# Kernel tuning notes

Measured on AMD Instinct MI355X. Metric: run time of the kernel, lower is better.

## Reference

```python
import jax, jax.numpy as jnp
import numpy as np

S = 64.0   # margin_loss scale
M2 = 0.5   # arcface additive angular margin (m1=1.0, m3=0.0)
EPS = 1e-7

BATCH = 1024
EMB = 512
NUM_CLASSES = 200000


def setup_inputs() -> dict:
    key = jax.random.key(0)
    k1, k2, k3 = jax.random.split(key, 3)
    embeddings = jax.random.normal(k1, (BATCH, EMB), dtype=jnp.float32)
    weight = jax.random.normal(k2, (NUM_CLASSES, EMB), dtype=jnp.float32) * 0.01
    labels = jax.random.randint(k3, (BATCH,), 0, NUM_CLASSES, dtype=jnp.int64)
    return {"embeddings": embeddings, "weight": weight, "labels": labels}


def reference(embeddings, weight, labels):
    # L2 normalize rows (torch.nn.functional.normalize, eps=1e-12)
    ne = embeddings / jnp.maximum(jnp.linalg.norm(embeddings, axis=1, keepdims=True), 1e-12)
    nw = weight / jnp.maximum(jnp.linalg.norm(weight, axis=1, keepdims=True), 1e-12)
    # cosine logits [B, C], clamped to [-1, 1]
    logits = jnp.clip(jnp.einsum('be,ce->bc', ne, nw), -1.0, 1.0)
    B = logits.shape[0]
    rows = jnp.arange(B)
    lbl = labels.astype(jnp.int32)
    # arcface margin: cos(theta + m2) applied only at the target class
    target = logits[rows, lbl]
    final_target = jnp.cos(jnp.arccos(jnp.clip(target, -1.0 + EPS, 1.0 - EPS)) + M2)
    logits = logits.at[rows, lbl].set(final_target) * S
    # mean cross-entropy
    logp = jax.nn.log_softmax(logits, axis=1)
    return -jnp.mean(logp[rows, lbl])
```

## Files before the change

### kernel.cpp

```cpp
#include <hip/hip_runtime.h>
#include <math.h>


#define S_SCALE 64.0f
#define MARGIN2 0.5f
#define EPSS 1e-7f

#define BATCH 1024
#define EMB 512
#define NCLS 200000

#define BM 256
#define BN 128
#define BK 32
#define NCHUNKS ((NCLS + BN - 1) / BN)
#define LDSTR 40

typedef __bf16 bf16x8 __attribute__((ext_vector_type(8)));
typedef float floatx4 __attribute__((ext_vector_type(4)));

#define OFF_NEBF 0
#define LEN_NEBF (BATCH * EMB / 2)
#define OFF_WINV (OFF_NEBF + LEN_NEBF)
#define LEN_WINV 200192
#define OFF_PM (OFF_WINV + LEN_WINV)
#define LEN_P (BATCH * NCHUNKS)
#define OFF_PL (OFF_PM + LEN_P)
#define OFF_TSV (OFF_PL + LEN_P)
#define OFF_RL (OFF_TSV + BATCH)

__device__ inline ushort f2bf(float f) {
    unsigned u = __float_as_uint(f);
    unsigned r = (u + 0x7FFFu + ((u >> 16) & 1u)) >> 16;
    return (ushort)r;
}

__global__ void norm_emb_kernel(const float* __restrict__ e, ushort* __restrict__ nebf) {
    int r = blockIdx.x;
    int t = threadIdx.x;
    float v0 = e[r * EMB + t];
    float v1 = e[r * EMB + t + 256];
    __shared__ float red[256];
    red[t] = v0 * v0 + v1 * v1;
    __syncthreads();
    for (int o = 128; o > 0; o >>= 1) {
        if (t < o) red[t] += red[t + o];
        __syncthreads();
    }
    float inv = 1.0f / fmaxf(sqrtf(red[0]), 1e-12f);
    nebf[r * EMB + t] = f2bf(v0 * inv);
    nebf[r * EMB + t + 256] = f2bf(v1 * inv);
}

__global__ void winv_kernel(const float* __restrict__ w, float* __restrict__ winv) {
    int tid = threadIdx.x;
    int wv = tid >> 6, lane = tid & 63;
    int row = blockIdx.x * 4 + wv;
    const float* wr = w + (size_t)row * EMB;
    float ss = 0.f;
#pragma unroll
    for (int q = 0; q < 8; ++q) {
        float v = wr[lane + 64 * q];
        ss += v * v;
    }
#pragma unroll
    for (int m = 32; m >= 1; m >>= 1) ss += __shfl_xor(ss, m);
    if (lane == 0) winv[row] = 1.0f / fmaxf(sqrtf(ss), 1e-12f);
}

__global__ __launch_bounds__(512) void gemm_lse_kernel(
    const ushort* __restrict__ nebf, const float* __restrict__ w,
    const float* __restrict__ winv, const int* __restrict__ labels,
    float* __restrict__ pm, float* __restrict__ pl, float* __restrict__ tsv) {
    __shared__ ushort Als[BM * LDSTR];
    __shared__ ushort Bls[BN * LDSTR];
    __shared__ float pmax[2][BM];
    __shared__ float psum[2][BM];

    const int tid = threadIdx.x;
    const int rowBase = blockIdx.x * BM;
    const int colBase = blockIdx.y * BN;
    const int lane = tid & 63, wv = tid >> 6;
    const int wm = wv & 3, wn = wv >> 1 & 0;
    (void)wm; (void)wn;
    const int wave_m = wv & 3, wave_n = wv >> 2;
    const int lr = lane & 15, quad = lane >> 4;

    const int arow = tid >> 1, ahalf = tid & 1;
    const int bcol = tid >> 2, bq = tid & 3;
    const int bcls = colBase + bcol;
    const bool bvalid = bcls < NCLS;

    floatx4 acc[4][4];
#pragma unroll
    for (int i = 0; i < 4; i++)
#pragma unroll
        for (int j = 0; j < 4; j++) acc[i][j] = (floatx4){0.f, 0.f, 0.f, 0.f};

    for (int kt = 0; kt < EMB; kt += BK) {
        {
            const ushort* src = nebf + (size_t)(rowBase + arow) * EMB + kt + ahalf * 16;
            uint4 v0 = *(const uint4*)(src);
            uint4 v1 = *(const uint4*)(src + 8);
            ushort* dst = &Als[arow * LDSTR + ahalf * 16];
            *(uint4*)(dst) = v0;
            *(uint4*)(dst + 8) = v1;
        }
        {
            float4 v0 = make_float4(0.f, 0.f, 0.f, 0.f);
            float4 v1 = make_float4(0.f, 0.f, 0.f, 0.f);
            if (bvalid) {
                const float* src = w + (size_t)bcls * EMB + kt + bq * 8;
                v0 = *(const float4*)(src);
                v1 = *(const float4*)(src + 4);
            }
            union { ushort us[8]; uint4 v; } pk;
            pk.us[0] = f2bf(v0.x); pk.us[1] = f2bf(v0.y);
            pk.us[2] = f2bf(v0.z); pk.us[3] = f2bf(v0.w);
            pk.us[4] = f2bf(v1.x); pk.us[5] = f2bf(v1.y);
            pk.us[6] = f2bf(v1.z); pk.us[7] = f2bf(v1.w);
            *(uint4*)&Bls[bcol * LDSTR + bq * 8] = pk.v;
        }
        __syncthreads();

        bf16x8 af[4], bfr[4];
#pragma unroll
        for (int i = 0; i < 4; i++)
            af[i] = *(const bf16x8*)&Als[(wave_m * 64 + i * 16 + lr) * LDSTR + quad * 8];
#pragma unroll
        for (int j = 0; j < 4; j++)
            bfr[j] = *(const bf16x8*)&Bls[(wave_n * 64 + j * 16 + lr) * LDSTR + quad * 8];
#pragma unroll
        for (int i = 0; i < 4; i++)
#pragma unroll
            for (int j = 0; j < 4; j++)
                acc[i][j] = __builtin_amdgcn_mfma_f32_16x16x32_bf16(af[i], bfr[j], acc[i][j], 0, 0, 0);
        __syncthreads();
    }

#pragma unroll
    for (int i = 0; i < 4; i++) {
#pragma unroll
        for (int r = 0; r < 4; r++) {
            int rowloc = wave_m * 64 + i * 16 + quad * 4 + r;
            int grow = rowBase + rowloc;
            int lbl = labels[grow];
            float vals[4];
            float vmax = -1e30f;
#pragma unroll
            for (int j = 0; j < 4; j++) {
                int gc = colBase + wave_n * 64 + j * 16 + lr;
                float v;
                if (gc < NCLS) {
                    v = acc[i][j][r] * winv[gc];
                    v = fminf(fmaxf(v, -1.f), 1.f);
                    if (gc == lbl) {
                        float tt = fminf(fmaxf(v, -1.f + EPSS), 1.f - EPSS);
                        v = __cosf(acosf(tt) + MARGIN2);
                        tsv[grow] = v * S_SCALE;
                    }
                    v *= S_SCALE;
                } else {
                    v = -1e30f;
                }
                vals[j] = v;
                vmax = fmaxf(vmax, v);
            }
#pragma unroll
            for (int m = 1; m < 16; m <<= 1) vmax = fmaxf(vmax, __shfl_xor(vmax, m));
            float s = 0.f;
#pragma unroll
            for (int j = 0; j < 4; j++) s += expf(vals[j] - vmax);
#pragma unroll
            for (int m = 1; m < 16; m <<= 1) s += __shfl_xor(s, m);
            if (lr == 0) {
                pmax[wave_n][rowloc] = vmax;
                psum[wave_n][rowloc] = s;
            }
        }
    }
    __syncthreads();
    if (tid < BM) {
        float m0 = pmax[0][tid], m1 = pmax[1][tid];
        float M = fmaxf(m0, m1);
        float l = psum[0][tid] * expf(m0 - M) + psum[1][tid] * expf(m1 - M);
        size_t grow = rowBase + tid;
        pm[grow * NCHUNKS + blockIdx.y] = M;
        pl[grow * NCHUNKS + blockIdx.y] = l;
    }
}

__global__ void chunk_reduce_kernel(const float* __restrict__ pm, const float* __restrict__ pl,
                                    const float* __restrict__ tsv, float* __restrict__ rowloss) {
    int r = blockIdx.x, t = threadIdx.x;
    const float* m = pm + (size_t)r * NCHUNKS;
    const float* l = pl + (size_t)r * NCHUNKS;
    __shared__ float red[256];
    float lmax = -1e30f;
    for (int i = t; i < NCHUNKS; i += 256) lmax = fmaxf(lmax, m[i]);
    red[t] = lmax;
    __syncthreads();
    for (int o = 128; o > 0; o >>= 1) {
        if (t < o) red[t] = fmaxf(red[t], red[t + o]);
        __syncthreads();
    }
    float M = red[0];
    __syncthreads();
    float s = 0.f;
    for (int i = t; i < NCHUNKS; i += 256) s += l[i] * expf(m[i] - M);
    red[t] = s;
    __syncthreads();
    for (int o = 128; o > 0; o >>= 1) {
        if (t < o) red[t] += red[t + o];
        __syncthreads();
    }
    if (t == 0) rowloss[r] = M + logf(red[0]) - tsv[r];
}

__global__ void final_kernel(const float* __restrict__ rowloss, float* __restrict__ out) {
    int t = threadIdx.x;
    float s = 0.f;
    for (int i = t; i < BATCH; i += 256) s += rowloss[i];
    __shared__ float red[256];
    red[t] = s;
    __syncthreads();
    for (int o = 128; o > 0; o >>= 1) {
        if (t < o) red[t] += red[t + o];
        __syncthreads();
    }
    if (t == 0) out[0] = red[0] / (float)BATCH;
}

extern "C" void kernel_launch(void* const* d_in, const int* in_sizes, int n_in,
                              void* d_out, int out_size, void* d_ws, size_t ws_size,
                              hipStream_t stream) {
    const float* emb = (const float*)d_in[0];
    const float* w = (const float*)d_in[1];
    const int* labels = (const int*)d_in[2];
    float* ws = (float*)d_ws;
    ushort* nebf = (ushort*)(ws + OFF_NEBF);
    float* winv = ws + OFF_WINV;
    float* pm = ws + OFF_PM;
    float* pl = ws + OFF_PL;
    float* tsv = ws + OFF_TSV;
    float* rl = ws + OFF_RL;

    norm_emb_kernel<<<BATCH, 256, 0, stream>>>(emb, nebf);
    winv_kernel<<<NCLS / 4, 256, 0, stream>>>(w, winv);
    dim3 grid(BATCH / BM, NCHUNKS);
    gemm_lse_kernel<<<grid, 512, 0, stream>>>(nebf, w, winv, labels, pm, pl, tsv);
    chunk_reduce_kernel<<<BATCH, 256, 0, stream>>>(pm, pl, tsv, rl);
    final_kernel<<<1, 256, 0, stream>>>(rl, (float*)d_out);
}
```

Baseline: 1.074 ms.

## Pre-normalize weights to bf16 and use fixed-max softmax bound

```diff
diff --git a/kernel.cpp b/kernel.cpp
--- a/kernel.cpp
+++ b/kernel.cpp
@@ -14,6 +14,7 @@
 #define BN 128
 #define BK 32
 #define NCHUNKS ((NCLS + BN - 1) / BN)
+#define NCLS_PAD (NCHUNKS * BN)
 #define LDSTR 40
 
 typedef __bf16 bf16x8 __attribute__((ext_vector_type(8)));
@@ -23,11 +24,13 @@
 #define LEN_NEBF (BATCH * EMB / 2)
 #define OFF_WINV (OFF_NEBF + LEN_NEBF)
 #define LEN_WINV 200192
-#define OFF_PM (OFF_WINV + LEN_WINV)
+#define OFF_PL (OFF_WINV + LEN_WINV)
 #define LEN_P (BATCH * NCHUNKS)
-#define OFF_PL (OFF_PM + LEN_P)
 #define OFF_TSV (OFF_PL + LEN_P)
 #define OFF_RL (OFF_TSV + BATCH)
+#define OFF_WBF (OFF_RL + BATCH)
+#define LEN_WBF ((size_t)NCLS_PAD * EMB / 2)
+#define NEED_BYTES (((size_t)OFF_WBF + LEN_WBF) * 4)
 
 __device__ inline ushort f2bf(float f) {
     unsigned u = __float_as_uint(f);
@@ -52,6 +55,28 @@
     nebf[r * EMB + t + 256] = f2bf(v1 * inv);
 }
 
+__global__ void norm_w_kernel(const float* __restrict__ w, ushort* __restrict__ wbf) {
+    int tid = threadIdx.x;
+    int wv = tid >> 6, lane = tid & 63;
+    int row = blockIdx.x * 4 + wv;
+    const float* wr = w + (size_t)row * EMB;
+    float4 v0 = *(const float4*)(wr + lane * 4);
+    float4 v1 = *(const float4*)(wr + lane * 4 + 256);
+    float ss = v0.x * v0.x + v0.y * v0.y + v0.z * v0.z + v0.w * v0.w
+             + v1.x * v1.x + v1.y * v1.y + v1.z * v1.z + v1.w * v1.w;
+#pragma unroll
+    for (int m = 32; m >= 1; m >>= 1) ss += __shfl_xor(ss, m);
+    float inv = 1.0f / fmaxf(sqrtf(ss), 1e-12f);
+    ushort* dst = wbf + (size_t)row * EMB;
+    ushort4 p0, p1;
+    p0.x = f2bf(v0.x * inv); p0.y = f2bf(v0.y * inv);
+    p0.z = f2bf(v0.z * inv); p0.w = f2bf(v0.w * inv);
+    p1.x = f2bf(v1.x * inv); p1.y = f2bf(v1.y * inv);
+    p1.z = f2bf(v1.z * inv); p1.w = f2bf(v1.w * inv);
+    *(ushort4*)(dst + lane * 4) = p0;
+    *(ushort4*)(dst + lane * 4 + 256) = p1;
+}
+
 __global__ void winv_kernel(const float* __restrict__ w, float* __restrict__ winv) {
     int tid = threadIdx.x;
     int wv = tid >> 6, lane = tid & 63;
@@ -68,21 +93,20 @@
     if (lane == 0) winv[row] = 1.0f / fmaxf(sqrtf(ss), 1e-12f);
 }
 
+template <bool PRE>
 __global__ __launch_bounds__(512) void gemm_lse_kernel(
-    const ushort* __restrict__ nebf, const float* __restrict__ w,
-    const float* __restrict__ winv, const int* __restrict__ labels,
-    float* __restrict__ pm, float* __restrict__ pl, float* __restrict__ tsv) {
+    const ushort* __restrict__ nebf, const ushort* __restrict__ wbf,
+    const float* __restrict__ w, const float* __restrict__ winv,
+    const int* __restrict__ labels,
+    float* __restrict__ pl, float* __restrict__ tsv) {
     __shared__ ushort Als[BM * LDSTR];
     __shared__ ushort Bls[BN * LDSTR];
-    __shared__ float pmax[2][BM];
     __shared__ float psum[2][BM];
 
     const int tid = threadIdx.x;
     const int rowBase = blockIdx.x * BM;
     const int colBase = blockIdx.y * BN;
     const int lane = tid & 63, wv = tid >> 6;
-    const int wm = wv & 3, wn = wv >> 1 & 0;
-    (void)wm; (void)wn;
     const int wave_m = wv & 3, wave_n = wv >> 2;
     const int lr = lane & 15, quad = lane >> 4;
 
@@ -106,7 +130,11 @@
             *(uint4*)(dst) = v0;
             *(uint4*)(dst + 8) = v1;
         }
-        {
+        if (PRE) {
+            uint4 v = make_uint4(0u, 0u, 0u, 0u);
+            if (bvalid) v = *(const uint4*)(wbf + (size_t)bcls * EMB + kt + bq * 8);
+            *(uint4*)&Bls[bcol * LDSTR + bq * 8] = v;
+        } else {
             float4 v0 = make_float4(0.f, 0.f, 0.f, 0.f);
             float4 v1 = make_float4(0.f, 0.f, 0.f, 0.f);
             if (bvalid) {
@@ -138,6 +166,14 @@
         __syncthreads();
     }
 
+    float wvv[4];
+    if (!PRE) {
+#pragma unroll
+        for (int j = 0; j < 4; j++) {
+            int gc = colBase + wave_n * 64 + j * 16 + lr;
+            wvv[j] = (gc < NCLS) ? winv[gc] : 0.f;
+        }
+    }
 #pragma unroll
     for (int i = 0; i < 4; i++) {
 #pragma unroll
@@ -145,76 +181,47 @@
             int rowloc = wave_m * 64 + i * 16 + quad * 4 + r;
             int grow = rowBase + rowloc;
             int lbl = labels[grow];
-            float vals[4];
-            float vmax = -1e30f;
+            float s = 0.f;
 #pragma unroll
             for (int j = 0; j < 4; j++) {
                 int gc = colBase + wave_n * 64 + j * 16 + lr;
-                float v;
                 if (gc < NCLS) {
-                    v = acc[i][j][r] * winv[gc];
-                    v = fminf(fmaxf(v, -1.f), 1.f);
+                    float c = PRE ? acc[i][j][r] : acc[i][j][r] * wvv[j];
+                    c = fminf(fmaxf(c, -1.f), 1.f);
                     if (gc == lbl) {
-                        float tt = fminf(fmaxf(v, -1.f + EPSS), 1.f - EPSS);
-                        v = __cosf(acosf(tt) + MARGIN2);
-                        tsv[grow] = v * S_SCALE;
+                        float tt = fminf(fmaxf(c, -1.f + EPSS), 1.f - EPSS);
+                        c = __cosf(acosf(tt) + MARGIN2);
+                        tsv[grow] = c * S_SCALE;
                     }
-                    v *= S_SCALE;
-                } else {
-                    v = -1e30f;
+                    s += expf(c * S_SCALE - S_SCALE);
                 }
-                vals[j] = v;
-                vmax = fmaxf(vmax, v);
             }
 #pragma unroll
-            for (int m = 1; m < 16; m <<= 1) vmax = fmaxf(vmax, __shfl_xor(vmax, m));
-            float s = 0.f;
-#pragma unroll
-            for (int j = 0; j < 4; j++) s += expf(vals[j] - vmax);
-#pragma unroll
             for (int m = 1; m < 16; m <<= 1) s += __shfl_xor(s, m);
-            if (lr == 0) {
-                pmax[wave_n][rowloc] = vmax;
-                psum[wave_n][rowloc] = s;
-            }
+            if (lr == 0) psum[wave_n][rowloc] = s;
         }
     }
     __syncthreads();
     if (tid < BM) {
-        float m0 = pmax[0][tid], m1 = pmax[1][tid];
-        float M = fmaxf(m0, m1);
-        float l = psum[0][tid] * expf(m0 - M) + psum[1][tid] * expf(m1 - M);
         size_t grow = rowBase + tid;
-        pm[grow * NCHUNKS + blockIdx.y] = M;
-        pl[grow * NCHUNKS + blockIdx.y] = l;
-    }
-}
-
-__global__ void chunk_reduce_kernel(const float* __restrict__ pm, const float* __restrict__ pl,
+        pl[grow * NCHUNKS + blockIdx.y] = psum[0][tid] + psum[1][tid];
+    }
+}
+
+__global__ void chunk_reduce_kernel(const float* __restrict__ pl,
                                     const float* __restrict__ tsv, float* __restrict__ rowloss) {
     int r = blockIdx.x, t = threadIdx.x;
-    const float* m = pm + (size_t)r * NCHUNKS;
     const float* l = pl + (size_t)r * NCHUNKS;
     __shared__ float red[256];
-    float lmax = -1e30f;
-    for (int i = t; i < NCHUNKS; i += 256) lmax = fmaxf(lmax, m[i]);
-    red[t] = lmax;
-    __syncthreads();
-    for (int o = 128; o > 0; o >>= 1) {
-        if (t < o) red[t] = fmaxf(red[t], red[t + o]);
-        __syncthreads();
-    }
-    float M = red[0];
-    __syncthreads();
     float s = 0.f;
-    for (int i = t; i < NCHUNKS; i += 256) s += l[i] * expf(m[i] - M);
+    for (int i = t; i < NCHUNKS; i += 256) s += l[i];
     red[t] = s;
     __syncthreads();
     for (int o = 128; o > 0; o >>= 1) {
         if (t < o) red[t] += red[t + o];
         __syncthreads();
     }
-    if (t == 0) rowloss[r] = M + logf(red[0]) - tsv[r];
+    if (t == 0) rowloss[r] = S_SCALE + logf(red[0]) - tsv[r];
 }
 
 __global__ void final_kernel(const float* __restrict__ rowloss, float* __restrict__ out) {
@@ -240,15 +247,22 @@
     float* ws = (float*)d_ws;
     ushort* nebf = (ushort*)(ws + OFF_NEBF);
     float* winv = ws + OFF_WINV;
-    float* pm = ws + OFF_PM;
     float* pl = ws + OFF_PL;
     float* tsv = ws + OFF_TSV;
     float* rl = ws + OFF_RL;
+    ushort* wbf = (ushort*)(ws + OFF_WBF);
+
+    const bool pre = ws_size >= NEED_BYTES;
 
     norm_emb_kernel<<<BATCH, 256, 0, stream>>>(emb, nebf);
-    winv_kernel<<<NCLS / 4, 256, 0, stream>>>(w, winv);
     dim3 grid(BATCH / BM, NCHUNKS);
-    gemm_lse_kernel<<<grid, 512, 0, stream>>>(nebf, w, winv, labels, pm, pl, tsv);
-    chunk_reduce_kernel<<<BATCH, 256, 0, stream>>>(pm, pl, tsv, rl);
+    if (pre) {
+        norm_w_kernel<<<NCLS / 4, 256, 0, stream>>>(w, wbf);
+        gemm_lse_kernel<true><<<grid, 512, 0, stream>>>(nebf, wbf, w, winv, labels, pl, tsv);
+    } else {
+        winv_kernel<<<NCLS / 4, 256, 0, stream>>>(w, winv);
+        gemm_lse_kernel<false><<<grid, 512, 0, stream>>>(nebf, wbf, w, winv, labels, pl, tsv);
+    }
+    chunk_reduce_kernel<<<BATCH, 256, 0, stream>>>(pl, tsv, rl);
     final_kernel<<<1, 256, 0, stream>>>(rl, (float*)d_out);
 }
```

New measurement: 955.7 us. 11.0% less time.
